# Kernel optimization log

Hardware: AMD Instinct MI355X
Metric: run time of the kernel (lower is better)

The kernel has to match this reference:

```python
import jax, jax.numpy as jnp
import numpy as np

ENC, TAG, LANG, ATT = 512, 512, 512, 256
N, P = 1024, 1024


def setup_inputs() -> dict:
    key = jax.random.key(0)
    ks = jax.random.split(key, 11)
    s = lambda d: 1.0 / np.sqrt(d)
    return {
        "encoder_out": jax.random.normal(ks[0], (1, P, ENC), jnp.float32),
        "decoder_hidden": jax.random.normal(ks[1], (N, TAG), jnp.float32),
        "language_out": jax.random.normal(ks[2], (N, LANG), jnp.float32),
        "We": jax.random.uniform(ks[3], (ATT, ENC), jnp.float32, -s(ENC), s(ENC)),
        "be": jax.random.uniform(ks[4], (ATT,), jnp.float32, -s(ENC), s(ENC)),
        "Wt": jax.random.uniform(ks[5], (ATT, TAG), jnp.float32, -s(TAG), s(TAG)),
        "bt": jax.random.uniform(ks[6], (ATT,), jnp.float32, -s(TAG), s(TAG)),
        "Wl": jax.random.uniform(ks[7], (ATT, LANG), jnp.float32, -s(LANG), s(LANG)),
        "bl": jax.random.uniform(ks[8], (ATT,), jnp.float32, -s(LANG), s(LANG)),
        "Wf": jax.random.uniform(ks[9], (1, ATT), jnp.float32, -s(ATT), s(ATT)),
        "bf": jax.random.uniform(ks[10], (1,), jnp.float32, -s(ATT), s(ATT)),
    }


def reference(encoder_out, decoder_hidden, language_out, We, be, Wt, bt, Wl, bl, Wf, bf):
    # att1: (1, P, A); att2, att3: (N, A)
    att1 = jnp.einsum("bpe,ae->bpa", encoder_out, We) + be
    att2 = decoder_hidden @ Wt.T + bt
    att3 = language_out @ Wl.T + bl
    # broadcast add -> (N, P, A), relu, reduce to scalar score per pixel
    h = jax.nn.relu(att1 + (att2 + att3)[:, None, :])  # (N, P, A)
    att = jnp.einsum("npa,a->np", h, Wf[0]) + bf[0]     # (N, P)
    alpha = jax.nn.softmax(att, axis=1)
    # softmax-weighted sum over pixels -> (N, ENC)
    awe = jnp.einsum("np,pe->ne", alpha, encoder_out[0])
    return awe, alpha
```

## Files before the change

### kernel.cpp

```cpp
#include <hip/hip_runtime.h>
#include <hip/hip_bf16.h>
#include <math.h>

#define ENC 512
#define ATT 256
#define NN 1024
#define PP 1024

typedef __attribute__((ext_vector_type(8))) __bf16 bf16x8;
typedef __attribute__((ext_vector_type(4))) float floatx4;
typedef __attribute__((ext_vector_type(2))) float floatx2;

union LdsVec { uint4 u; bf16x8 v; };

__device__ __forceinline__ unsigned cvt_pk(float lo, float hi) {
    union { __hip_bfloat162 h; unsigned u; } x;
    x.h = __float22bfloat162_rn(float2{lo, hi});
    return x.u;
}
__device__ __forceinline__ uint4 cvt8(float4 f0, float4 f1) {
    uint4 r;
    r.x = cvt_pk(f0.x, f0.y); r.y = cvt_pk(f0.z, f0.w);
    r.z = cvt_pk(f1.x, f1.y); r.w = cvt_pk(f1.z, f1.w);
    return r;
}

__device__ __forceinline__ int t64_off(int row, int k) {
    return row * 64 + ((((k >> 3) ^ row) & 7) << 3) + (k & 7);
}

__global__ __launch_bounds__(256) void mfma_uv(
    const float* __restrict__ E,  const float* __restrict__ We, const float* __restrict__ be,
    const float* __restrict__ D,  const float* __restrict__ Wt, const float* __restrict__ bt,
    const float* __restrict__ Lg, const float* __restrict__ Wl, const float* __restrict__ bl,
    float* __restrict__ uT, float* __restrict__ v1T, float* __restrict__ v2T,
    unsigned short* __restrict__ ET)
{
    const int tid = threadIdx.x;

    if (blockIdx.z == 3) {
        __shared__ unsigned short T[64][72];
        const int k0 = blockIdx.y * 64;
        const int kr = tid >> 2, nc = (tid & 3) * 16;
        const int nr = tid >> 2, kc = (tid & 3) * 16;
        #pragma unroll
        for (int t = 0; t < 2; ++t) {
            const int n0 = (blockIdx.x * 2 + t) * 64;
            const float* ep = E + (size_t)(k0 + kr) * ENC + n0 + nc;
            float4 a = *(const float4*)(ep + 0),  b = *(const float4*)(ep + 4);
            float4 c = *(const float4*)(ep + 8),  d = *(const float4*)(ep + 12);
            if (t) __syncthreads();
            *(uint4*)&T[kr][nc]     = cvt8(a, b);
            *(uint4*)&T[kr][nc + 8] = cvt8(c, d);
            __syncthreads();
            unsigned short tmp[16];
            #pragma unroll
            for (int i = 0; i < 16; ++i) tmp[i] = T[kc + i][nr];
            unsigned short* op = ET + (size_t)(n0 + nr) * PP + k0 + kc;
            *(uint4*)(op)     = *(uint4*)&tmp[0];
            *(uint4*)(op + 8) = *(uint4*)&tmp[8];
        }
        return;
    }

    __shared__ __align__(16) unsigned short As[2][64 * 64];
    __shared__ __align__(16) unsigned short Bs[2][64 * 64];
    const int K = 512;

    const float *A, *B, *bias; float* out;
    if      (blockIdx.z == 0) { A = E;  B = We; bias = be; out = uT;  }
    else if (blockIdx.z == 1) { A = D;  B = Wt; bias = bt; out = v1T; }
    else                      { A = Lg; B = Wl; bias = bl; out = v2T; }

    const int m0 = blockIdx.y * 64, n0 = blockIdx.x * 64;
    const int wv = tid >> 6, lm = tid & 15, lq = (tid >> 4) & 3;
    const int mb = (wv & 1) * 32, nb = (wv >> 1) * 32;
    const int a0l = t64_off(mb + lm,      lq * 8),      a0h = t64_off(mb + lm,      lq * 8 + 32);
    const int a1l = t64_off(mb + 16 + lm, lq * 8),      a1h = t64_off(mb + 16 + lm, lq * 8 + 32);
    const int b0l = t64_off(nb + lm,      lq * 8),      b0h = t64_off(nb + lm,      lq * 8 + 32);
    const int b1l = t64_off(nb + 16 + lm, lq * 8),      b1h = t64_off(nb + 16 + lm, lq * 8 + 32);

    const int row = tid >> 2, kseg = tid & 3;
    const int s0 = t64_off(row, kseg * 8);
    const int s1 = t64_off(row, kseg * 8 + 32);
    const float* Ap = A + (size_t)(m0 + row) * K + kseg * 8;
    const float* Bp = B + (size_t)(n0 + row) * K + kseg * 8;

    floatx4 acc[2][2];
    const floatx4 zero = {0.f, 0.f, 0.f, 0.f};
    acc[0][0] = zero; acc[0][1] = zero; acc[1][0] = zero; acc[1][1] = zero;

    float4 pa0 = *(const float4*)(Ap),      pa1 = *(const float4*)(Ap + 4);
    float4 pa2 = *(const float4*)(Ap + 32), pa3 = *(const float4*)(Ap + 36);
    float4 pb0 = *(const float4*)(Bp),      pb1 = *(const float4*)(Bp + 4);
    float4 pb2 = *(const float4*)(Bp + 32), pb3 = *(const float4*)(Bp + 36);

    for (int k0 = 0; k0 < K; k0 += 64) {
        const int buf = (k0 >> 6) & 1;
        *(uint4*)&As[buf][s0] = cvt8(pa0, pa1);
        *(uint4*)&As[buf][s1] = cvt8(pa2, pa3);
        *(uint4*)&Bs[buf][s0] = cvt8(pb0, pb1);
        *(uint4*)&Bs[buf][s1] = cvt8(pb2, pb3);
        __syncthreads();
        if (k0 + 64 < K) {
            pa0 = *(const float4*)(Ap + k0 + 64); pa1 = *(const float4*)(Ap + k0 + 68);
            pa2 = *(const float4*)(Ap + k0 + 96); pa3 = *(const float4*)(Ap + k0 + 100);
            pb0 = *(const float4*)(Bp + k0 + 64); pb1 = *(const float4*)(Bp + k0 + 68);
            pb2 = *(const float4*)(Bp + k0 + 96); pb3 = *(const float4*)(Bp + k0 + 100);
        }
        LdsVec fa0l, fa0h, fa1l, fa1h, fb0l, fb0h, fb1l, fb1h;
        fa0l.u = *(const uint4*)&As[buf][a0l];  fa0h.u = *(const uint4*)&As[buf][a0h];
        fa1l.u = *(const uint4*)&As[buf][a1l];  fa1h.u = *(const uint4*)&As[buf][a1h];
        fb0l.u = *(const uint4*)&Bs[buf][b0l];  fb0h.u = *(const uint4*)&Bs[buf][b0h];
        fb1l.u = *(const uint4*)&Bs[buf][b1l];  fb1h.u = *(const uint4*)&Bs[buf][b1h];
        acc[0][0] = __builtin_amdgcn_mfma_f32_16x16x32_bf16(fa0l.v, fb0l.v, acc[0][0], 0, 0, 0);
        acc[0][1] = __builtin_amdgcn_mfma_f32_16x16x32_bf16(fa0l.v, fb1l.v, acc[0][1], 0, 0, 0);
        acc[1][0] = __builtin_amdgcn_mfma_f32_16x16x32_bf16(fa1l.v, fb0l.v, acc[1][0], 0, 0, 0);
        acc[1][1] = __builtin_amdgcn_mfma_f32_16x16x32_bf16(fa1l.v, fb1l.v, acc[1][1], 0, 0, 0);
        acc[0][0] = __builtin_amdgcn_mfma_f32_16x16x32_bf16(fa0h.v, fb0h.v, acc[0][0], 0, 0, 0);
        acc[0][1] = __builtin_amdgcn_mfma_f32_16x16x32_bf16(fa0h.v, fb1h.v, acc[0][1], 0, 0, 0);
        acc[1][0] = __builtin_amdgcn_mfma_f32_16x16x32_bf16(fa1h.v, fb0h.v, acc[1][0], 0, 0, 0);
        acc[1][1] = __builtin_amdgcn_mfma_f32_16x16x32_bf16(fa1h.v, fb1h.v, acc[1][1], 0, 0, 0);
    }

    #pragma unroll
    for (int s = 0; s < 2; ++s) {
        const int col = n0 + nb + s * 16 + lm;
        const float bsum = bias[col];
        #pragma unroll
        for (int t = 0; t < 2; ++t) {
            const int mbase = m0 + mb + t * 16 + lq * 4;
            float4 o;
            o.x = acc[t][s][0] + bsum; o.y = acc[t][s][1] + bsum;
            o.z = acc[t][s][2] + bsum; o.w = acc[t][s][3] + bsum;
            *(float4*)&out[(size_t)col * NN + mbase] = o;
        }
    }
}

__global__ __launch_bounds__(256) void att_fused(
    const float* __restrict__ uT, const float* __restrict__ v1T,
    const float* __restrict__ v2T,
    const float* __restrict__ Wf, float* __restrict__ att_part)
{
    __shared__ float us[32][68];
    __shared__ float vs[32][68];
    __shared__ float wfs[128];
    const int tid = threadIdx.x;
    const int z = blockIdx.z;
    if (tid < 128) wfs[tid] = Wf[z * 128 + tid];
    const int p0 = blockIdx.x * 64, n0 = blockIdx.y * 64;
    const int rowS = tid >> 3, cS = (tid & 7) * 8;
    const int tx = tid & 15, ty = tid >> 4;

    floatx2 acc[4][2];
    const floatx2 z2 = {0.f, 0.f};
    #pragma unroll
    for (int j = 0; j < 4; ++j) { acc[j][0] = z2; acc[j][1] = z2; }

    const int abase = z * 128;
    for (int ac = 0; ac < 128; ac += 32) {
        __syncthreads();
        {
            const float* up = &uT[(size_t)(abase + ac + rowS) * NN + p0 + cS];
            float4 f0 = *(const float4*)up;
            float4 f1 = *(const float4*)(up + 4);
            *(float4*)&us[rowS][cS]     = f0;
            *(float4*)&us[rowS][cS + 4] = f1;
            const size_t vidx = (size_t)(abase + ac + rowS) * NN + n0 + cS;
            float4 g0 = *(const float4*)&v1T[vidx];
            float4 g1 = *(const float4*)&v1T[vidx + 4];
            float4 h0 = *(const float4*)&v2T[vidx];
            float4 h1 = *(const float4*)&v2T[vidx + 4];
            float4 s0, s1;
            s0.x = g0.x + h0.x; s0.y = g0.y + h0.y; s0.z = g0.z + h0.z; s0.w = g0.w + h0.w;
            s1.x = g1.x + h1.x; s1.y = g1.y + h1.y; s1.z = g1.z + h1.z; s1.w = g1.w + h1.w;
            *(float4*)&vs[rowS][cS]     = s0;
            *(float4*)&vs[rowS][cS + 4] = s1;
        }
        __syncthreads();
        #pragma unroll
        for (int a4 = 0; a4 < 32; a4 += 4) {
            float4 w4 = *(const float4*)&wfs[ac + a4];
            #pragma unroll
            for (int aa = 0; aa < 4; ++aa) {
                const int a = a4 + aa;
                float4 u4 = *(const float4*)&us[a][tx * 4];
                float4 v4 = *(const float4*)&vs[a][ty * 4];
                const float w = (aa == 0) ? w4.x : (aa == 1) ? w4.y : (aa == 2) ? w4.z : w4.w;
                floatx2 ulo = {u4.x, u4.y}, uhi = {u4.z, u4.w};
                const float vv[4] = {v4.x, v4.y, v4.z, v4.w};
                #pragma unroll
                for (int j = 0; j < 4; ++j) {
                    floatx2 t0 = ulo + vv[j];
                    floatx2 t1 = uhi + vv[j];
                    t0 = __builtin_elementwise_max(t0, z2);
                    t1 = __builtin_elementwise_max(t1, z2);
                    acc[j][0] = t0 * w + acc[j][0];
                    acc[j][1] = t1 * w + acc[j][1];
                }
            }
        }
    }

    float* outp = att_part + (size_t)z * NN * PP;
    #pragma unroll
    for (int j = 0; j < 4; ++j) {
        float4 o;
        o.x = acc[j][0].x; o.y = acc[j][0].y; o.z = acc[j][1].x; o.w = acc[j][1].y;
        *(float4*)&outp[(size_t)(n0 + ty * 4 + j) * PP + p0 + tx * 4] = o;
    }
}

__global__ __launch_bounds__(256) void softmax_rows(
    const float* __restrict__ att_part, float* __restrict__ alpha,
    unsigned short* __restrict__ alpha_bf)
{
    const int wv = threadIdx.x >> 6, lane = threadIdx.x & 63;
    const int n = blockIdx.x * 4 + wv;
    const float* r0 = att_part + (size_t)n * PP;
    const float* r1 = att_part + (size_t)NN * PP + (size_t)n * PP;

    float4 x[4];
    #pragma unroll
    for (int i = 0; i < 4; ++i) {
        float4 a = *(const float4*)&r0[i * 256 + lane * 4];
        float4 b = *(const float4*)&r1[i * 256 + lane * 4];
        x[i].x = a.x + b.x; x[i].y = a.y + b.y; x[i].z = a.z + b.z; x[i].w = a.w + b.w;
    }

    float m = -1e30f;
    #pragma unroll
    for (int i = 0; i < 4; ++i)
        m = fmaxf(m, fmaxf(fmaxf(x[i].x, x[i].y), fmaxf(x[i].z, x[i].w)));
    #pragma unroll
    for (int off = 32; off > 0; off >>= 1) m = fmaxf(m, __shfl_xor(m, off, 64));

    float s = 0.f;
    #pragma unroll
    for (int i = 0; i < 4; ++i) {
        x[i].x = __expf(x[i].x - m); x[i].y = __expf(x[i].y - m);
        x[i].z = __expf(x[i].z - m); x[i].w = __expf(x[i].w - m);
        s += x[i].x + x[i].y + x[i].z + x[i].w;
    }
    #pragma unroll
    for (int off = 32; off > 0; off >>= 1) s += __shfl_xor(s, off, 64);
    const float inv = 1.0f / s;

    float* ar = alpha + (size_t)n * PP;
    unsigned short* br = alpha_bf + (size_t)n * PP;
    #pragma unroll
    for (int i = 0; i < 4; ++i) {
        x[i].x *= inv; x[i].y *= inv; x[i].z *= inv; x[i].w *= inv;
        *(float4*)&ar[i * 256 + lane * 4] = x[i];
        uint2 pk;
        pk.x = cvt_pk(x[i].x, x[i].y);
        pk.y = cvt_pk(x[i].z, x[i].w);
        *(uint2*)&br[i * 256 + lane * 4] = pk;
    }
}

__global__ __launch_bounds__(256) void mfma_awe(
    const unsigned short* __restrict__ alpha_bf,
    const unsigned short* __restrict__ ET, float* __restrict__ awe)
{
    __shared__ __align__(16) unsigned short As[2][32 * 64];
    __shared__ __align__(16) unsigned short Bs[2][64 * 64];
    const int tid = threadIdx.x;
    const int K = PP;
    const int m0 = blockIdx.y * 32, n0 = blockIdx.x * 64;
    const int wv = tid >> 6, lm = tid & 15, lq = (tid >> 4) & 3;
    const int mw = (wv & 1) * 16, nw = (wv >> 1) * 32;
    const int aol = t64_off(mw + lm,      lq * 8),  aoh = t64_off(mw + lm,      lq * 8 + 32);
    const int b0l = t64_off(nw + lm,      lq * 8),  b0h = t64_off(nw + lm,      lq * 8 + 32);
    const int b1l = t64_off(nw + 16 + lm, lq * 8),  b1h = t64_off(nw + 16 + lm, lq * 8 + 32);

    const int rowA = tid >> 3, kcA = (tid & 7) * 8;
    const int rowB = tid >> 2, kcB = (tid & 3) * 8;
    const int aoff  = t64_off(rowA, kcA);
    const int boff0 = t64_off(rowB, kcB);
    const int boff1 = t64_off(rowB, kcB + 32);
    const unsigned short* Ap = alpha_bf + (size_t)(m0 + rowA) * PP + kcA;
    const unsigned short* Bp = ET + (size_t)(n0 + rowB) * PP + kcB;

    floatx4 acc[2];
    const floatx4 zero = {0.f, 0.f, 0.f, 0.f};
    acc[0] = zero; acc[1] = zero;

    uint4 pa  = *(const uint4*)Ap;
    uint4 pb0 = *(const uint4*)Bp;
    uint4 pb1 = *(const uint4*)(Bp + 32);

    for (int k0 = 0; k0 < K; k0 += 64) {
        const int buf = (k0 >> 6) & 1;
        *(uint4*)&As[buf][aoff]  = pa;
        *(uint4*)&Bs[buf][boff0] = pb0;
        *(uint4*)&Bs[buf][boff1] = pb1;
        __syncthreads();
        if (k0 + 64 < K) {
            pa  = *(const uint4*)(Ap + k0 + 64);
            pb0 = *(const uint4*)(Bp + k0 + 64);
            pb1 = *(const uint4*)(Bp + k0 + 96);
        }
        LdsVec fal, fah, fb0l, fb0h, fb1l, fb1h;
        fal.u  = *(const uint4*)&As[buf][aol];
        fah.u  = *(const uint4*)&As[buf][aoh];
        fb0l.u = *(const uint4*)&Bs[buf][b0l];
        fb0h.u = *(const uint4*)&Bs[buf][b0h];
        fb1l.u = *(const uint4*)&Bs[buf][b1l];
        fb1h.u = *(const uint4*)&Bs[buf][b1h];
        acc[0] = __builtin_amdgcn_mfma_f32_16x16x32_bf16(fal.v, fb0l.v, acc[0], 0, 0, 0);
        acc[1] = __builtin_amdgcn_mfma_f32_16x16x32_bf16(fal.v, fb1l.v, acc[1], 0, 0, 0);
        acc[0] = __builtin_amdgcn_mfma_f32_16x16x32_bf16(fah.v, fb0h.v, acc[0], 0, 0, 0);
        acc[1] = __builtin_amdgcn_mfma_f32_16x16x32_bf16(fah.v, fb1h.v, acc[1], 0, 0, 0);
    }

    #pragma unroll
    for (int s = 0; s < 2; ++s) {
        const int col = n0 + nw + s * 16 + lm;
        #pragma unroll
        for (int r = 0; r < 4; ++r)
            awe[(size_t)(m0 + mw + lq * 4 + r) * ENC + col] = acc[s][r];
    }
}

extern "C" void kernel_launch(void* const* d_in, const int* in_sizes, int n_in,
                              void* d_out, int out_size, void* d_ws, size_t ws_size,
                              hipStream_t stream)
{
    const float* encoder = (const float*)d_in[0];
    const float* dec     = (const float*)d_in[1];
    const float* lang    = (const float*)d_in[2];
    const float* We      = (const float*)d_in[3];
    const float* be      = (const float*)d_in[4];
    const float* Wt      = (const float*)d_in[5];
    const float* bt      = (const float*)d_in[6];
    const float* Wl      = (const float*)d_in[7];
    const float* bl      = (const float*)d_in[8];
    const float* Wf      = (const float*)d_in[9];

    float* uT   = (float*)d_ws;
    float* v1T  = uT  + ATT * NN;
    float* v2T  = v1T + ATT * NN;
    float* attp = v2T + ATT * NN;
    unsigned short* alpha_bf = (unsigned short*)(attp + 2 * (size_t)NN * PP);
    unsigned short* ET       = alpha_bf + (size_t)NN * PP;

    float* awe   = (float*)d_out;
    float* alpha = (float*)d_out + NN * ENC;

    mfma_uv<<<dim3(4, 16, 4), 256, 0, stream>>>(
        encoder, We, be, dec, Wt, bt, lang, Wl, bl, uT, v1T, v2T, ET);
    att_fused<<<dim3(PP / 64, NN / 64, 2), 256, 0, stream>>>(uT, v1T, v2T, Wf, attp);
    softmax_rows<<<dim3(NN / 4), 256, 0, stream>>>(attp, alpha, alpha_bf);
    mfma_awe<<<dim3(ENC / 64, NN / 32), 256, 0, stream>>>(alpha_bf, ET, awe);
}
```

Before: 123.2 us.

## Fuse row softmax into awe GEMM, keeping alpha tile in LDS

```diff
diff --git a/kernel.cpp b/kernel.cpp
--- a/kernel.cpp
+++ b/kernel.cpp
@@ -27,6 +27,9 @@
 
 __device__ __forceinline__ int t64_off(int row, int k) {
     return row * 64 + ((((k >> 3) ^ row) & 7) << 3) + (k & 7);
+}
+__device__ __forceinline__ int al_off(int c, int row, int k) {
+    return c * 2048 + row * 64 + ((((k >> 3) ^ row ^ c) & 7) << 3) + (k & 7);
 }
 
 __global__ __launch_bounds__(256) void mfma_uv(
@@ -212,99 +215,99 @@
     }
 }
 
-__global__ __launch_bounds__(256) void softmax_rows(
-    const float* __restrict__ att_part, float* __restrict__ alpha,
-    unsigned short* __restrict__ alpha_bf)
+__global__ __launch_bounds__(256) void softmax_awe(
+    const float* __restrict__ att_part, const unsigned short* __restrict__ ET,
+    float* __restrict__ alpha, float* __restrict__ awe)
 {
-    const int wv = threadIdx.x >> 6, lane = threadIdx.x & 63;
-    const int n = blockIdx.x * 4 + wv;
-    const float* r0 = att_part + (size_t)n * PP;
-    const float* r1 = att_part + (size_t)NN * PP + (size_t)n * PP;
-
-    float4 x[4];
-    #pragma unroll
-    for (int i = 0; i < 4; ++i) {
-        float4 a = *(const float4*)&r0[i * 256 + lane * 4];
-        float4 b = *(const float4*)&r1[i * 256 + lane * 4];
-        x[i].x = a.x + b.x; x[i].y = a.y + b.y; x[i].z = a.z + b.z; x[i].w = a.w + b.w;
-    }
-
-    float m = -1e30f;
-    #pragma unroll
-    for (int i = 0; i < 4; ++i)
-        m = fmaxf(m, fmaxf(fmaxf(x[i].x, x[i].y), fmaxf(x[i].z, x[i].w)));
-    #pragma unroll
-    for (int off = 32; off > 0; off >>= 1) m = fmaxf(m, __shfl_xor(m, off, 64));
-
-    float s = 0.f;
-    #pragma unroll
-    for (int i = 0; i < 4; ++i) {
-        x[i].x = __expf(x[i].x - m); x[i].y = __expf(x[i].y - m);
-        x[i].z = __expf(x[i].z - m); x[i].w = __expf(x[i].w - m);
-        s += x[i].x + x[i].y + x[i].z + x[i].w;
-    }
-    #pragma unroll
-    for (int off = 32; off > 0; off >>= 1) s += __shfl_xor(s, off, 64);
-    const float inv = 1.0f / s;
-
-    float* ar = alpha + (size_t)n * PP;
-    unsigned short* br = alpha_bf + (size_t)n * PP;
-    #pragma unroll
-    for (int i = 0; i < 4; ++i) {
-        x[i].x *= inv; x[i].y *= inv; x[i].z *= inv; x[i].w *= inv;
-        *(float4*)&ar[i * 256 + lane * 4] = x[i];
-        uint2 pk;
-        pk.x = cvt_pk(x[i].x, x[i].y);
-        pk.y = cvt_pk(x[i].z, x[i].w);
-        *(uint2*)&br[i * 256 + lane * 4] = pk;
-    }
-}
-
-__global__ __launch_bounds__(256) void mfma_awe(
-    const unsigned short* __restrict__ alpha_bf,
-    const unsigned short* __restrict__ ET, float* __restrict__ awe)
-{
-    __shared__ __align__(16) unsigned short As[2][32 * 64];
+    __shared__ __align__(16) unsigned short Al[16 * 2048];
     __shared__ __align__(16) unsigned short Bs[2][64 * 64];
     const int tid = threadIdx.x;
-    const int K = PP;
-    const int m0 = blockIdx.y * 32, n0 = blockIdx.x * 64;
+    const int bid = blockIdx.x;
+    const int by = bid & 31, bx = bid >> 5;
+    const int m0 = by * 32, n0 = bx * 64;
+
+    const int rowB = tid >> 2, kcB = (tid & 3) * 8;
+    const int boff0 = t64_off(rowB, kcB);
+    const int boff1 = t64_off(rowB, kcB + 32);
+    const unsigned short* Bp = ET + (size_t)(n0 + rowB) * PP + kcB;
+    uint4 pb0 = *(const uint4*)Bp;
+    uint4 pb1 = *(const uint4*)(Bp + 32);
+
+    const int sub = tid & 31;
+    const int rsub = tid >> 5;
+    #pragma unroll
+    for (int g = 0; g < 4; ++g) {
+        const int r = g * 8 + rsub;
+        const float* p0 = att_part + (size_t)(m0 + r) * PP + sub * 32;
+        const float* p1 = p0 + (size_t)NN * PP;
+        float4 x[8];
+        #pragma unroll
+        for (int j = 0; j < 8; ++j) {
+            float4 a = *(const float4*)(p0 + j * 4);
+            float4 b = *(const float4*)(p1 + j * 4);
+            x[j].x = a.x + b.x; x[j].y = a.y + b.y;
+            x[j].z = a.z + b.z; x[j].w = a.w + b.w;
+        }
+        float m = -1e30f;
+        #pragma unroll
+        for (int j = 0; j < 8; ++j)
+            m = fmaxf(m, fmaxf(fmaxf(x[j].x, x[j].y), fmaxf(x[j].z, x[j].w)));
+        #pragma unroll
+        for (int off = 16; off > 0; off >>= 1) m = fmaxf(m, __shfl_xor(m, off, 64));
+        float s = 0.f;
+        #pragma unroll
+        for (int j = 0; j < 8; ++j) {
+            x[j].x = __expf(x[j].x - m); x[j].y = __expf(x[j].y - m);
+            x[j].z = __expf(x[j].z - m); x[j].w = __expf(x[j].w - m);
+            s += (x[j].x + x[j].y) + (x[j].z + x[j].w);
+        }
+        #pragma unroll
+        for (int off = 16; off > 0; off >>= 1) s += __shfl_xor(s, off, 64);
+        const float inv = 1.0f / s;
+        #pragma unroll
+        for (int j = 0; j < 8; ++j) {
+            x[j].x *= inv; x[j].y *= inv; x[j].z *= inv; x[j].w *= inv;
+        }
+        if (bx == 0) {
+            float* ar = alpha + (size_t)(m0 + r) * PP + sub * 32;
+            #pragma unroll
+            for (int j = 0; j < 8; ++j) *(float4*)(ar + j * 4) = x[j];
+        }
+        #pragma unroll
+        for (int j8 = 0; j8 < 4; ++j8) {
+            const int p = sub * 32 + j8 * 8;
+            const int c = p >> 6, kin = p & 63;
+            uint4 u;
+            u.x = cvt_pk(x[2 * j8].x,     x[2 * j8].y);
+            u.y = cvt_pk(x[2 * j8].z,     x[2 * j8].w);
+            u.z = cvt_pk(x[2 * j8 + 1].x, x[2 * j8 + 1].y);
+            u.w = cvt_pk(x[2 * j8 + 1].z, x[2 * j8 + 1].w);
+            *(uint4*)&Al[al_off(c, r, kin)] = u;
+        }
+    }
+    __syncthreads();
+
     const int wv = tid >> 6, lm = tid & 15, lq = (tid >> 4) & 3;
     const int mw = (wv & 1) * 16, nw = (wv >> 1) * 32;
-    const int aol = t64_off(mw + lm,      lq * 8),  aoh = t64_off(mw + lm,      lq * 8 + 32);
     const int b0l = t64_off(nw + lm,      lq * 8),  b0h = t64_off(nw + lm,      lq * 8 + 32);
     const int b1l = t64_off(nw + 16 + lm, lq * 8),  b1h = t64_off(nw + 16 + lm, lq * 8 + 32);
-
-    const int rowA = tid >> 3, kcA = (tid & 7) * 8;
-    const int rowB = tid >> 2, kcB = (tid & 3) * 8;
-    const int aoff  = t64_off(rowA, kcA);
-    const int boff0 = t64_off(rowB, kcB);
-    const int boff1 = t64_off(rowB, kcB + 32);
-    const unsigned short* Ap = alpha_bf + (size_t)(m0 + rowA) * PP + kcA;
-    const unsigned short* Bp = ET + (size_t)(n0 + rowB) * PP + kcB;
 
     floatx4 acc[2];
     const floatx4 zero = {0.f, 0.f, 0.f, 0.f};
     acc[0] = zero; acc[1] = zero;
 
-    uint4 pa  = *(const uint4*)Ap;
-    uint4 pb0 = *(const uint4*)Bp;
-    uint4 pb1 = *(const uint4*)(Bp + 32);
-
-    for (int k0 = 0; k0 < K; k0 += 64) {
-        const int buf = (k0 >> 6) & 1;
-        *(uint4*)&As[buf][aoff]  = pa;
+    for (int c = 0; c < 16; ++c) {
+        const int buf = c & 1;
         *(uint4*)&Bs[buf][boff0] = pb0;
         *(uint4*)&Bs[buf][boff1] = pb1;
         __syncthreads();
-        if (k0 + 64 < K) {
-            pa  = *(const uint4*)(Ap + k0 + 64);
-            pb0 = *(const uint4*)(Bp + k0 + 64);
-            pb1 = *(const uint4*)(Bp + k0 + 96);
+        if (c + 1 < 16) {
+            pb0 = *(const uint4*)(Bp + (c + 1) * 64);
+            pb1 = *(const uint4*)(Bp + (c + 1) * 64 + 32);
         }
         LdsVec fal, fah, fb0l, fb0h, fb1l, fb1h;
-        fal.u  = *(const uint4*)&As[buf][aol];
-        fah.u  = *(const uint4*)&As[buf][aoh];
+        fal.u  = *(const uint4*)&Al[al_off(c, mw + lm, lq * 8)];
+        fah.u  = *(const uint4*)&Al[al_off(c, mw + lm, lq * 8 + 32)];
         fb0l.u = *(const uint4*)&Bs[buf][b0l];
         fb0h.u = *(const uint4*)&Bs[buf][b0h];
         fb1l.u = *(const uint4*)&Bs[buf][b1l];
@@ -313,6 +316,7 @@
         acc[1] = __builtin_amdgcn_mfma_f32_16x16x32_bf16(fal.v, fb1l.v, acc[1], 0, 0, 0);
         acc[0] = __builtin_amdgcn_mfma_f32_16x16x32_bf16(fah.v, fb0h.v, acc[0], 0, 0, 0);
         acc[1] = __builtin_amdgcn_mfma_f32_16x16x32_bf16(fah.v, fb1h.v, acc[1], 0, 0, 0);
+        __syncthreads();
     }
 
     #pragma unroll
@@ -343,8 +347,7 @@
     float* v1T  = uT  + ATT * NN;
     float* v2T  = v1T + ATT * NN;
     float* attp = v2T + ATT * NN;
-    unsigned short* alpha_bf = (unsigned short*)(attp + 2 * (size_t)NN * PP);
-    unsigned short* ET       = alpha_bf + (size_t)NN * PP;
+    unsigned short* ET = (unsigned short*)(attp + 2 * (size_t)NN * PP);
 
     float* awe   = (float*)d_out;
     float* alpha = (float*)d_out + NN * ENC;
@@ -352,6 +355,5 @@
     mfma_uv<<<dim3(4, 16, 4), 256, 0, stream>>>(
         encoder, We, be, dec, Wt, bt, lang, Wl, bl, uT, v1T, v2T, ET);
     att_fused<<<dim3(PP / 64, NN / 64, 2), 256, 0, stream>>>(uT, v1T, v2T, Wf, attp);
-    softmax_rows<<<dim3(NN / 4), 256, 0, stream>>>(attp, alpha, alpha_bf);
-    mfma_awe<<<dim3(ENC / 64, NN / 32), 256, 0, stream>>>(alpha_bf, ET, awe);
-}
+    softmax_awe<<<dim3(256), 256, 0, stream>>>(attp, ET, alpha, awe);
+}
```

Measured after the change: 133.5 us. 8.3% more time.

## Fuse softmax into score and awe kernels using unnormalized exp with atomic row sums

Applied to the files above, without the earlier changes.

```diff
diff --git a/kernel.cpp b/kernel.cpp
--- a/kernel.cpp
+++ b/kernel.cpp
@@ -34,11 +34,12 @@
     const float* __restrict__ D,  const float* __restrict__ Wt, const float* __restrict__ bt,
     const float* __restrict__ Lg, const float* __restrict__ Wl, const float* __restrict__ bl,
     float* __restrict__ uT, float* __restrict__ v1T, float* __restrict__ v2T,
-    unsigned short* __restrict__ ET)
+    unsigned short* __restrict__ ET, float* __restrict__ srow)
 {
     const int tid = threadIdx.x;
 
     if (blockIdx.z == 3) {
+        if (blockIdx.y == 0) srow[blockIdx.x * 256 + tid] = 0.f;
         __shared__ unsigned short T[64][72];
         const int k0 = blockIdx.y * 64;
         const int kr = tid >> 2, nc = (tid & 3) * 16;
@@ -138,45 +139,37 @@
     }
 }
 
-__global__ __launch_bounds__(256) void att_fused(
+__global__ __launch_bounds__(256) void att_exp(
     const float* __restrict__ uT, const float* __restrict__ v1T,
-    const float* __restrict__ v2T,
-    const float* __restrict__ Wf, float* __restrict__ att_part)
+    const float* __restrict__ v2T, const float* __restrict__ Wf,
+    float* __restrict__ expv, unsigned short* __restrict__ exp_bf,
+    float* __restrict__ srow)
 {
     __shared__ float us[32][68];
-    __shared__ float vs[32][68];
-    __shared__ float wfs[128];
+    __shared__ float vs[32][36];
+    __shared__ __align__(16) float wfs[256];
     const int tid = threadIdx.x;
-    const int z = blockIdx.z;
-    if (tid < 128) wfs[tid] = Wf[z * 128 + tid];
-    const int p0 = blockIdx.x * 64, n0 = blockIdx.y * 64;
-    const int rowS = tid >> 3, cS = (tid & 7) * 8;
+    wfs[tid] = Wf[tid];
+    const int p0 = blockIdx.x * 64, n0 = blockIdx.y * 32;
+    const int rowS = tid >> 3, cS = (tid & 7) * 8, cV = (tid & 7) * 4;
     const int tx = tid & 15, ty = tid >> 4;
 
-    floatx2 acc[4][2];
+    floatx2 aL[2], aH[2];
     const floatx2 z2 = {0.f, 0.f};
-    #pragma unroll
-    for (int j = 0; j < 4; ++j) { acc[j][0] = z2; acc[j][1] = z2; }
-
-    const int abase = z * 128;
-    for (int ac = 0; ac < 128; ac += 32) {
+    aL[0] = z2; aL[1] = z2; aH[0] = z2; aH[1] = z2;
+
+    for (int ac = 0; ac < 256; ac += 32) {
         __syncthreads();
         {
-            const float* up = &uT[(size_t)(abase + ac + rowS) * NN + p0 + cS];
-            float4 f0 = *(const float4*)up;
-            float4 f1 = *(const float4*)(up + 4);
-            *(float4*)&us[rowS][cS]     = f0;
-            *(float4*)&us[rowS][cS + 4] = f1;
-            const size_t vidx = (size_t)(abase + ac + rowS) * NN + n0 + cS;
-            float4 g0 = *(const float4*)&v1T[vidx];
-            float4 g1 = *(const float4*)&v1T[vidx + 4];
-            float4 h0 = *(const float4*)&v2T[vidx];
-            float4 h1 = *(const float4*)&v2T[vidx + 4];
-            float4 s0, s1;
-            s0.x = g0.x + h0.x; s0.y = g0.y + h0.y; s0.z = g0.z + h0.z; s0.w = g0.w + h0.w;
-            s1.x = g1.x + h1.x; s1.y = g1.y + h1.y; s1.z = g1.z + h1.z; s1.w = g1.w + h1.w;
-            *(float4*)&vs[rowS][cS]     = s0;
-            *(float4*)&vs[rowS][cS + 4] = s1;
+            const float* up = &uT[(size_t)(ac + rowS) * NN + p0 + cS];
+            *(float4*)&us[rowS][cS]     = *(const float4*)up;
+            *(float4*)&us[rowS][cS + 4] = *(const float4*)(up + 4);
+            const size_t vidx = (size_t)(ac + rowS) * NN + n0 + cV;
+            float4 g = *(const float4*)&v1T[vidx];
+            float4 h = *(const float4*)&v2T[vidx];
+            float4 sv;
+            sv.x = g.x + h.x; sv.y = g.y + h.y; sv.z = g.z + h.z; sv.w = g.w + h.w;
+            *(float4*)&vs[rowS][cV] = sv;
         }
         __syncthreads();
         #pragma unroll
@@ -186,89 +179,55 @@
             for (int aa = 0; aa < 4; ++aa) {
                 const int a = a4 + aa;
                 float4 u4 = *(const float4*)&us[a][tx * 4];
-                float4 v4 = *(const float4*)&vs[a][ty * 4];
+                float2 vv = *(const float2*)&vs[a][ty * 2];
                 const float w = (aa == 0) ? w4.x : (aa == 1) ? w4.y : (aa == 2) ? w4.z : w4.w;
                 floatx2 ulo = {u4.x, u4.y}, uhi = {u4.z, u4.w};
-                const float vv[4] = {v4.x, v4.y, v4.z, v4.w};
-                #pragma unroll
-                for (int j = 0; j < 4; ++j) {
-                    floatx2 t0 = ulo + vv[j];
-                    floatx2 t1 = uhi + vv[j];
-                    t0 = __builtin_elementwise_max(t0, z2);
-                    t1 = __builtin_elementwise_max(t1, z2);
-                    acc[j][0] = t0 * w + acc[j][0];
-                    acc[j][1] = t1 * w + acc[j][1];
-                }
+                floatx2 t0, t1;
+                t0 = ulo + vv.x; t1 = uhi + vv.x;
+                t0 = __builtin_elementwise_max(t0, z2);
+                t1 = __builtin_elementwise_max(t1, z2);
+                aL[0] = t0 * w + aL[0];
+                aH[0] = t1 * w + aH[0];
+                t0 = ulo + vv.y; t1 = uhi + vv.y;
+                t0 = __builtin_elementwise_max(t0, z2);
+                t1 = __builtin_elementwise_max(t1, z2);
+                aL[1] = t0 * w + aL[1];
+                aH[1] = t1 * w + aH[1];
             }
         }
     }
 
-    float* outp = att_part + (size_t)z * NN * PP;
     #pragma unroll
-    for (int j = 0; j < 4; ++j) {
-        float4 o;
-        o.x = acc[j][0].x; o.y = acc[j][0].y; o.z = acc[j][1].x; o.w = acc[j][1].y;
-        *(float4*)&outp[(size_t)(n0 + ty * 4 + j) * PP + p0 + tx * 4] = o;
-    }
-}
-
-__global__ __launch_bounds__(256) void softmax_rows(
-    const float* __restrict__ att_part, float* __restrict__ alpha,
-    unsigned short* __restrict__ alpha_bf)
-{
-    const int wv = threadIdx.x >> 6, lane = threadIdx.x & 63;
-    const int n = blockIdx.x * 4 + wv;
-    const float* r0 = att_part + (size_t)n * PP;
-    const float* r1 = att_part + (size_t)NN * PP + (size_t)n * PP;
-
-    float4 x[4];
-    #pragma unroll
-    for (int i = 0; i < 4; ++i) {
-        float4 a = *(const float4*)&r0[i * 256 + lane * 4];
-        float4 b = *(const float4*)&r1[i * 256 + lane * 4];
-        x[i].x = a.x + b.x; x[i].y = a.y + b.y; x[i].z = a.z + b.z; x[i].w = a.w + b.w;
-    }
-
-    float m = -1e30f;
-    #pragma unroll
-    for (int i = 0; i < 4; ++i)
-        m = fmaxf(m, fmaxf(fmaxf(x[i].x, x[i].y), fmaxf(x[i].z, x[i].w)));
-    #pragma unroll
-    for (int off = 32; off > 0; off >>= 1) m = fmaxf(m, __shfl_xor(m, off, 64));
-
-    float s = 0.f;
-    #pragma unroll
-    for (int i = 0; i < 4; ++i) {
-        x[i].x = __expf(x[i].x - m); x[i].y = __expf(x[i].y - m);
-        x[i].z = __expf(x[i].z - m); x[i].w = __expf(x[i].w - m);
-        s += x[i].x + x[i].y + x[i].z + x[i].w;
-    }
-    #pragma unroll
-    for (int off = 32; off > 0; off >>= 1) s += __shfl_xor(s, off, 64);
-    const float inv = 1.0f / s;
-
-    float* ar = alpha + (size_t)n * PP;
-    unsigned short* br = alpha_bf + (size_t)n * PP;
-    #pragma unroll
-    for (int i = 0; i < 4; ++i) {
-        x[i].x *= inv; x[i].y *= inv; x[i].z *= inv; x[i].w *= inv;
-        *(float4*)&ar[i * 256 + lane * 4] = x[i];
+    for (int j = 0; j < 2; ++j) {
+        const int n = n0 + ty * 2 + j;
+        float4 ex;
+        ex.x = __expf(aL[j][0]); ex.y = __expf(aL[j][1]);
+        ex.z = __expf(aH[j][0]); ex.w = __expf(aH[j][1]);
+        float psum = (ex.x + ex.y) + (ex.z + ex.w);
+        psum += __shfl_xor(psum, 1, 64);
+        psum += __shfl_xor(psum, 2, 64);
+        psum += __shfl_xor(psum, 4, 64);
+        psum += __shfl_xor(psum, 8, 64);
+        if (tx == 0) atomicAdd(&srow[n], psum);
+        *(float4*)&expv[(size_t)n * PP + p0 + tx * 4] = ex;
         uint2 pk;
-        pk.x = cvt_pk(x[i].x, x[i].y);
-        pk.y = cvt_pk(x[i].z, x[i].w);
-        *(uint2*)&br[i * 256 + lane * 4] = pk;
-    }
-}
-
-__global__ __launch_bounds__(256) void mfma_awe(
-    const unsigned short* __restrict__ alpha_bf,
-    const unsigned short* __restrict__ ET, float* __restrict__ awe)
+        pk.x = cvt_pk(ex.x, ex.y); pk.y = cvt_pk(ex.z, ex.w);
+        *(uint2*)&exp_bf[(size_t)n * PP + p0 + tx * 4] = pk;
+    }
+}
+
+__global__ __launch_bounds__(256) void awe_alpha(
+    const unsigned short* __restrict__ exp_bf, const unsigned short* __restrict__ ET,
+    const float* __restrict__ expv, const float* __restrict__ srow,
+    float* __restrict__ alpha, float* __restrict__ awe)
 {
     __shared__ __align__(16) unsigned short As[2][32 * 64];
     __shared__ __align__(16) unsigned short Bs[2][64 * 64];
     const int tid = threadIdx.x;
+    const int bid = blockIdx.x;
+    const int by = bid & 31, bx = bid >> 5;
     const int K = PP;
-    const int m0 = blockIdx.y * 32, n0 = blockIdx.x * 64;
+    const int m0 = by * 32, n0 = bx * 64;
     const int wv = tid >> 6, lm = tid & 15, lq = (tid >> 4) & 3;
     const int mw = (wv & 1) * 16, nw = (wv >> 1) * 32;
     const int aol = t64_off(mw + lm,      lq * 8),  aoh = t64_off(mw + lm,      lq * 8 + 32);
@@ -280,7 +239,7 @@
     const int aoff  = t64_off(rowA, kcA);
     const int boff0 = t64_off(rowB, kcB);
     const int boff1 = t64_off(rowB, kcB + 32);
-    const unsigned short* Ap = alpha_bf + (size_t)(m0 + rowA) * PP + kcA;
+    const unsigned short* Ap = exp_bf + (size_t)(m0 + rowA) * PP + kcA;
     const unsigned short* Bp = ET + (size_t)(n0 + rowB) * PP + kcB;
 
     floatx4 acc[2];
@@ -313,14 +272,32 @@
         acc[1] = __builtin_amdgcn_mfma_f32_16x16x32_bf16(fal.v, fb1l.v, acc[1], 0, 0, 0);
         acc[0] = __builtin_amdgcn_mfma_f32_16x16x32_bf16(fah.v, fb0h.v, acc[0], 0, 0, 0);
         acc[1] = __builtin_amdgcn_mfma_f32_16x16x32_bf16(fah.v, fb1h.v, acc[1], 0, 0, 0);
-    }
-
+        __syncthreads();
+    }
+
+    float invr[4];
+    #pragma unroll
+    for (int r = 0; r < 4; ++r) invr[r] = 1.0f / srow[m0 + mw + lq * 4 + r];
     #pragma unroll
     for (int s = 0; s < 2; ++s) {
         const int col = n0 + nw + s * 16 + lm;
         #pragma unroll
         for (int r = 0; r < 4; ++r)
-            awe[(size_t)(m0 + mw + lq * 4 + r) * ENC + col] = acc[s][r];
+            awe[(size_t)(m0 + mw + lq * 4 + r) * ENC + col] = acc[s][r] * invr[r];
+    }
+
+    {
+        const int arow = m0 + (tid >> 3);
+        const int acol = bx * 128 + (tid & 7) * 16;
+        const float inv = 1.0f / srow[arow];
+        const float* src = expv + (size_t)arow * PP + acol;
+        float* dst = alpha + (size_t)arow * PP + acol;
+        #pragma unroll
+        for (int q = 0; q < 4; ++q) {
+            float4 x = *(const float4*)(src + q * 4);
+            x.x *= inv; x.y *= inv; x.z *= inv; x.w *= inv;
+            *(float4*)(dst + q * 4) = x;
+        }
     }
 }
 
@@ -342,16 +319,17 @@
     float* uT   = (float*)d_ws;
     float* v1T  = uT  + ATT * NN;
     float* v2T  = v1T + ATT * NN;
-    float* attp = v2T + ATT * NN;
-    unsigned short* alpha_bf = (unsigned short*)(attp + 2 * (size_t)NN * PP);
-    unsigned short* ET       = alpha_bf + (size_t)NN * PP;
+    float* expv = v2T + ATT * NN;
+    float* srow = expv + (size_t)NN * PP;
+    unsigned short* exp_bf = (unsigned short*)(srow + NN);
+    unsigned short* ET     = exp_bf + (size_t)NN * PP;
 
     float* awe   = (float*)d_out;
     float* alpha = (float*)d_out + NN * ENC;
 
     mfma_uv<<<dim3(4, 16, 4), 256, 0, stream>>>(
-        encoder, We, be, dec, Wt, bt, lang, Wl, bl, uT, v1T, v2T, ET);
-    att_fused<<<dim3(PP / 64, NN / 64, 2), 256, 0, stream>>>(uT, v1T, v2T, Wf, attp);
-    softmax_rows<<<dim3(NN / 4), 256, 0, stream>>>(attp, alpha, alpha_bf);
-    mfma_awe<<<dim3(ENC / 64, NN / 32), 256, 0, stream>>>(alpha_bf, ET, awe);
-}
+        encoder, We, be, dec, Wt, bt, lang, Wl, bl, uT, v1T, v2T, ET, srow);
+    att_exp<<<dim3(PP / 64, NN / 32), 256, 0, stream>>>(
+        uT, v1T, v2T, Wf, expv, exp_bf, srow);
+    awe_alpha<<<dim3(256), 256, 0, stream>>>(exp_bf, ET, expv, srow, alpha, awe);
+}
```

After: 126.0 us. +2.2%, slower.
